# Optimization experiments

Hardware: AMD Instinct MI355X
Metric: run time of the kernel (lower is better)

Reference implementation:

```python
import jax, jax.numpy as jnp
import numpy as np
from jax import lax

# dims per init_kwargs / input_specs
V, D, N, W, B, T = 32000, 512, 250000, 64, 4, 1024
LOOPS, THRESH = 4, 0.99


def _ln(x, scale, bias):
    m = jnp.mean(x, -1, keepdims=True)
    v = jnp.var(x, -1, keepdims=True)
    return (x - m) * lax.rsqrt(v + 1e-5) * scale + bias


def setup_inputs() -> dict:
    key = jax.random.key(0)
    ks = jax.random.split(key, 12)
    s = 0.02
    p = lambda k, shape: jax.random.normal(k, shape, jnp.float32) * s
    return {
        "input_ids": jax.random.randint(ks[0], (B, T), 0, V),
        "embed": p(ks[1], (V, D)),
        "enc_w": p(ks[2], (D, D)), "enc_b": jnp.zeros((D,), jnp.float32),
        "ln_enc_s": jnp.ones((D,), jnp.float32), "ln_enc_b": jnp.zeros((D,), jnp.float32),
        "idx_w": p(ks[3], (D, D)), "idx_b": jnp.zeros((D,), jnp.float32),
        "mu_w": p(ks[4], (D, 1)), "mu_b": jnp.zeros((1,), jnp.float32),
        "sig_w": p(ks[5], (D, 1)), "sig_b": jnp.zeros((1,), jnp.float32),
        "pool_table": p(ks[6], (N, D)),
        "int_w1": p(ks[7], (2 * D, D)), "int_b1": jnp.zeros((D,), jnp.float32),
        "int_w2": p(ks[8], (D, D)), "int_b2": jnp.zeros((D,), jnp.float32),
        "ln_s": jnp.ones((D,), jnp.float32), "ln_b": jnp.zeros((D,), jnp.float32),
        "halt_w": p(ks[9], (D, 1)), "halt_b": jnp.zeros((1,), jnp.float32),
        "dec_w": p(ks[10], (D, V)), "dec_b": jnp.zeros((V,), jnp.float32),
    }


def reference(input_ids, embed, enc_w, enc_b, ln_enc_s, ln_enc_b,
              idx_w, idx_b, mu_w, mu_b, sig_w, sig_b, pool_table,
              int_w1, int_b1, int_w2, int_b2, ln_s, ln_b,
              halt_w, halt_b, dec_w, dec_b):
    # TinyController.encode: embed -> Dense -> gelu -> LayerNorm
    hidden = _ln(jax.nn.gelu(embed[input_ids] @ enc_w + enc_b), ln_enc_s, ln_enc_b)  # [B,T,D]
    state = hidden
    dt = hidden.dtype
    halt_prob = jnp.zeros((B, T, 1), dt)
    halted = jnp.zeros((B, T, 1), dt)
    idxs = []
    for _ in range(LOOPS):  # fixed small loop count, unrolled
        prev = state
        pooled = jnp.mean(state, axis=1)                       # [B,D]
        h = jax.nn.gelu(pooled @ idx_w + idx_b)
        mu = jax.nn.sigmoid(h @ mu_w + mu_b)                   # [B,1], coord in [0,1]
        sigma = jax.nn.softplus(h @ sig_w + sig_b) + 1e-4      # [B,1]
        # CoordinateMassivePool: contiguous window of W rows around mu*N
        center = mu[:, 0] * N
        start = jnp.clip(jnp.floor(center - W / 2).astype(jnp.int32), 0, N - W)  # [B]
        window = jax.vmap(lambda s: lax.dynamic_slice(pool_table, (s, 0), (W, D)))(start)  # [B,W,D]
        pos = (start[:, None] + jnp.arange(W)[None, :]).astype(dt) / N            # [B,W]
        w = jnp.exp(-0.5 * ((pos - mu) / sigma) ** 2)
        w = w / jnp.sum(w, axis=-1, keepdims=True)
        retrieved = jnp.einsum('bw,bwd->bd', w, window)        # [B,D]
        combined = jnp.concatenate(
            [state, jnp.broadcast_to(retrieved[:, None, :], (B, T, D))], axis=-1)  # [B,T,2D]
        integrated = _ln(jax.nn.gelu(combined @ int_w1 + int_b1) @ int_w2 + int_b2, ln_s, ln_b)
        candidate = state + integrated
        # ACT halting
        p_halt = jax.nn.sigmoid(candidate @ halt_w + halt_b)   # [B,T,1]
        halt_prob = halt_prob + p_halt * (1.0 - halted)
        new_halted = (halt_prob > THRESH).astype(dt)
        state = (1.0 - halted) * candidate + halted * prev
        halted = new_halted
        idxs.append(start)
    logits = state @ dec_w + dec_b                             # [B,T,V]
    all_indices = jnp.stack(idxs, axis=1)                      # [B,LOOPS]
    return logits, all_indices
```

## Files before the change

kernel.cpp:

```cpp
#include <hip/hip_runtime.h>

#define DEV __device__ __forceinline__

typedef __attribute__((ext_vector_type(8))) short bf16x8;
typedef __attribute__((ext_vector_type(4))) float f32x4;

typedef const __attribute__((address_space(1))) void* gsrc_t;
typedef __attribute__((address_space(3))) void* gdst_t;

DEV void gld16(const void* g, void* l){ __builtin_amdgcn_global_load_lds((gsrc_t)g,(gdst_t)l,16,0,0); }

DEV unsigned short f2bf(float f){
  union { float f; unsigned int u; } x; x.f = f;
  unsigned int u = x.u;
  return (unsigned short)((u + 0x7fffu + ((u >> 16) & 1u)) >> 16);
}
DEV unsigned long long pack4bf(float a, float b, float c, float d){
  return (unsigned long long)f2bf(a)
       | ((unsigned long long)f2bf(b) << 16)
       | ((unsigned long long)f2bf(c) << 32)
       | ((unsigned long long)f2bf(d) << 48);
}
DEV float gelu_t(float x){
  float u = 0.7978845608028654f * (x + 0.044715f * x * x * x);
  return 0.5f * x * (1.0f + tanhf(u));
}
DEV float sigmoidf_(float x){ return 1.0f / (1.0f + expf(-x)); }

DEV void BAR_TOP(){ __builtin_amdgcn_s_barrier(); asm volatile("" ::: "memory"); }
DEV void BAR_END(){
  __builtin_amdgcn_sched_barrier(0);
  asm volatile("s_waitcnt lgkmcnt(0)" ::: "memory");
  __builtin_amdgcn_s_barrier();
  asm volatile("" ::: "memory");
}

__global__ __launch_bounds__(256) void kPrep(const float* __restrict__ dec_w,
                                             unsigned short* __restrict__ dec_wT,
                                             const float* __restrict__ s0, const float* __restrict__ s1,
                                             const float* __restrict__ s2,
                                             unsigned short* __restrict__ d0, unsigned short* __restrict__ d1,
                                             unsigned short* __restrict__ d2,
                                             const int* __restrict__ ids,
                                             const float* __restrict__ embed,
                                             unsigned short* __restrict__ E){
  __shared__ float t[64][65];
  const int bid = blockIdx.x, tid = threadIdx.x;
  if (bid < 4000){
    int n0 = (bid % 500) * 64, k0 = (bid / 500) * 64;
    #pragma unroll
    for (int i = 0; i < 16; i++){
      int idx = i * 256 + tid; int r = idx >> 6, c = idx & 63;
      t[r][c] = dec_w[(size_t)(k0 + r) * 32000 + n0 + c];
    }
    __syncthreads();
    #pragma unroll
    for (int i = 0; i < 16; i++){
      int idx = i * 256 + tid; int r = idx >> 6, c = idx & 63;
      dec_wT[(size_t)(n0 + r) * 512 + k0 + c] = f2bf(t[c][r]);
    }
  } else if (bid < 4192){
    int rel = bid - 4000;
    int z = rel >> 6, rem = rel & 63;
    const float* W = (z == 0) ? s0 : (z == 1) ? s1 : s2;
    unsigned short* D = (z == 0) ? d0 : (z == 1) ? d1 : d2;
    int n0 = (rem & 7) * 64, k0 = (rem >> 3) * 64;
    #pragma unroll
    for (int i = 0; i < 16; i++){
      int idx = i * 256 + tid; int r = idx >> 6, c = idx & 63;
      t[r][c] = W[(size_t)(k0 + r) * 512 + n0 + c];
    }
    __syncthreads();
    #pragma unroll
    for (int i = 0; i < 16; i++){
      int idx = i * 256 + tid; int r = idx >> 6, c = idx & 63;
      D[(size_t)(n0 + r) * 512 + k0 + c] = f2bf(t[c][r]);
    }
  } else {
    int idx = bid - 4192;
    int row = idx * 2 + (tid >> 7);
    int t2  = tid & 127;
    int id = ids[row];
    float4 v = ((const float4*)(embed + (size_t)id * 512))[t2];
    *(unsigned long long*)(E + (size_t)row * 512 + t2 * 4) = pack4bf(v.x, v.y, v.z, v.w);
  }
}

template<int ENC>
__global__ __launch_bounds__(512) void kGemmLN(
    const unsigned short* __restrict__ A, const unsigned short* __restrict__ BT,
    const float* __restrict__ bias, const float* __restrict__ lns, const float* __restrict__ lnb,
    const float* __restrict__ hw, const float* __restrict__ hb,
    float* __restrict__ st, unsigned short* __restrict__ stb,
    float* __restrict__ part, float* __restrict__ halt_p, float* __restrict__ halted){
  __shared__ alignas(16) unsigned short lA[2][16 * 32];
  __shared__ alignas(16) unsigned short lB[2][512 * 32];
  __shared__ float pS[8][16], pQ[8][16], pH[8][16];
  __shared__ float sMean[16], sRs[16], sFac[16];
  const int tid = threadIdx.x, w = tid >> 6, lane = tid & 63;
  const int q = lane >> 4, c = lane & 15, lk8 = q * 8;
  const int r0 = blockIdx.x * 16;
  const int br = tid >> 2, bk = (tid & 3) * 8;
  f32x4 acc[4] = {};

  auto STAGE = [&](int buf, int k0){
    if (w == 0)
      gld16(A + (size_t)(r0 + (lane >> 2)) * 512 + k0 + (lane & 3) * 8, &lA[buf][lane * 8]);
    #pragma unroll
    for (int i = 0; i < 4; i++)
      gld16(BT + (size_t)(i * 128 + br) * 512 + k0 + bk, &lB[buf][(i * 512 + tid) * 8]);
  };

  STAGE(0, 0);
  #pragma unroll
  for (int t = 0; t < 16; t++){
    if (t < 15){
      STAGE((t + 1) & 1, (t + 1) * 32);
      if (w == 0) asm volatile("s_waitcnt vmcnt(5)" ::: "memory");
      else        asm volatile("s_waitcnt vmcnt(4)" ::: "memory");
    } else {
      asm volatile("s_waitcnt vmcnt(0)" ::: "memory");
    }
    BAR_TOP();
    bf16x8 af = *(const bf16x8*)&lA[t & 1][c * 32 + lk8];
    bf16x8 bfv[4];
    #pragma unroll
    for (int n = 0; n < 4; n++)
      bfv[n] = *(const bf16x8*)&lB[t & 1][(w * 64 + n * 16 + c) * 32 + lk8];
    #pragma unroll
    for (int n = 0; n < 4; n++)
      acc[n] = __builtin_amdgcn_mfma_f32_16x16x32_bf16(af, bfv[n], acc[n], 0, 0, 0);
    BAR_END();
  }

  #pragma unroll
  for (int n = 0; n < 4; n++){
    float bcol = bias[w * 64 + n * 16 + c];
    #pragma unroll
    for (int r = 0; r < 4; r++){
      float v = acc[n][r] + bcol;
      if (ENC) v = gelu_t(v);
      acc[n][r] = v;
    }
  }
  float rS[4], rQ[4];
  #pragma unroll
  for (int r = 0; r < 4; r++){
    float s = 0.f, s2 = 0.f;
    #pragma unroll
    for (int n = 0; n < 4; n++){ float v = acc[n][r]; s += v; s2 += v * v; }
    rS[r] = s; rQ[r] = s2;
  }
  #pragma unroll
  for (int mask = 1; mask < 16; mask <<= 1)
    #pragma unroll
    for (int r = 0; r < 4; r++){
      rS[r] += __shfl_xor(rS[r], mask);
      rQ[r] += __shfl_xor(rQ[r], mask);
    }
  if (c == 0)
    #pragma unroll
    for (int r = 0; r < 4; r++){ pS[w][q * 4 + r] = rS[r]; pQ[w][q * 4 + r] = rQ[r]; }
  __syncthreads();
  if (tid < 16){
    float s = 0.f, s2 = 0.f;
    #pragma unroll
    for (int v = 0; v < 8; v++){ s += pS[v][tid]; s2 += pQ[v][tid]; }
    float mean = s * (1.f / 512.f);
    float var  = s2 * (1.f / 512.f) - mean * mean;
    sMean[tid] = mean; sRs[tid] = rsqrtf(var + 1e-5f);
    if (ENC){ halt_p[r0 + tid] = 0.f; halted[r0 + tid] = 0.f; }
  }
  __syncthreads();
  float lnsv[4], lnbv[4];
  #pragma unroll
  for (int n = 0; n < 4; n++){ lnsv[n] = lns[w * 64 + n * 16 + c]; lnbv[n] = lnb[w * 64 + n * 16 + c]; }
  #pragma unroll
  for (int r = 0; r < 4; r++){
    int row = q * 4 + r;
    float mu = sMean[row], rs = sRs[row];
    #pragma unroll
    for (int n = 0; n < 4; n++)
      acc[n][r] = (acc[n][r] - mu) * rs * lnsv[n] + lnbv[n];
  }

  float sold[4][4];
  if (!ENC){
    float hwv[4];
    #pragma unroll
    for (int n = 0; n < 4; n++) hwv[n] = hw[w * 64 + n * 16 + c];
    #pragma unroll
    for (int r = 0; r < 4; r++){
      int row = q * 4 + r;
      #pragma unroll
      for (int n = 0; n < 4; n++)
        sold[n][r] = st[(size_t)(r0 + row) * 512 + w * 64 + n * 16 + c];
    }
    float rH[4];
    #pragma unroll
    for (int r = 0; r < 4; r++){
      float d = 0.f;
      #pragma unroll
      for (int n = 0; n < 4; n++) d += (sold[n][r] + acc[n][r]) * hwv[n];
      rH[r] = d;
    }
    #pragma unroll
    for (int mask = 1; mask < 16; mask <<= 1)
      #pragma unroll
      for (int r = 0; r < 4; r++) rH[r] += __shfl_xor(rH[r], mask);
    if (c == 0)
      #pragma unroll
      for (int r = 0; r < 4; r++) pH[w][q * 4 + r] = rH[r];
    __syncthreads();
    if (tid < 16){
      float d = 0.f;
      #pragma unroll
      for (int v = 0; v < 8; v++) d += pH[v][tid];
      float hd = halted[r0 + tid];
      float p  = sigmoidf_(d + hb[0]);
      float hp = halt_p[r0 + tid] + p * (1.f - hd);
      halt_p[r0 + tid] = hp;
      halted[r0 + tid] = (hp > 0.99f) ? 1.f : 0.f;
      sFac[tid] = 1.f - hd;
    }
    __syncthreads();
    #pragma unroll
    for (int r = 0; r < 4; r++){
      float f = sFac[q * 4 + r];
      #pragma unroll
      for (int n = 0; n < 4; n++)
        acc[n][r] = sold[n][r] + f * acc[n][r];
    }
  }

  #pragma unroll
  for (int r = 0; r < 4; r++){
    int row = r0 + q * 4 + r;
    #pragma unroll
    for (int n = 0; n < 4; n++){
      int col = w * 64 + n * 16 + c;
      float v = acc[n][r];
      st [(size_t)row * 512 + col] = v;
      stb[(size_t)row * 512 + col] = f2bf(v);
    }
  }
  #pragma unroll
  for (int n = 0; n < 4; n++){
    float s = 0.f;
    #pragma unroll
    for (int r = 0; r < 4; r++) s += acc[n][r];
    s += __shfl_xor(s, 16);
    s += __shfl_xor(s, 32);
    if (q == 0) part[(size_t)blockIdx.x * 512 + w * 64 + n * 16 + c] = s;
  }
}

__global__ __launch_bounds__(256) void kGemm64(const unsigned short* __restrict__ A,
                                               const unsigned short* __restrict__ BT,
                                               const float* __restrict__ rb,
                                               unsigned short* __restrict__ C){
  __shared__ alignas(16) unsigned short lA[2][64 * 32];
  __shared__ alignas(16) unsigned short lB[2][64 * 32];
  const int tid = threadIdx.x, w = tid >> 6, lane = tid & 63;
  const int q = lane >> 4, c = lane & 15, lk8 = q * 8;
  const int wm = w >> 1, wn = w & 1;
  const int m0 = blockIdx.y * 64, n0 = blockIdx.x * 64;
  const int sr = tid >> 2, sk = (tid & 3) * 8;
  f32x4 acc[2][2] = {};

  auto STAGE = [&](int buf, int k0){
    gld16(A  + (size_t)(m0 + sr) * 512 + k0 + sk, &lA[buf][tid * 8]);
    gld16(BT + (size_t)(n0 + sr) * 512 + k0 + sk, &lB[buf][tid * 8]);
  };

  STAGE(0, 0);
  #pragma unroll
  for (int t = 0; t < 16; t++){
    if (t < 15){
      STAGE((t + 1) & 1, (t + 1) * 32);
      asm volatile("s_waitcnt vmcnt(2)" ::: "memory");
    } else {
      asm volatile("s_waitcnt vmcnt(0)" ::: "memory");
    }
    BAR_TOP();
    bf16x8 af[2], bfv[2];
    #pragma unroll
    for (int m = 0; m < 2; m++) af[m]  = *(const bf16x8*)&lA[t & 1][(wm * 32 + m * 16 + c) * 32 + lk8];
    #pragma unroll
    for (int n = 0; n < 2; n++) bfv[n] = *(const bf16x8*)&lB[t & 1][(wn * 32 + n * 16 + c) * 32 + lk8];
    #pragma unroll
    for (int m = 0; m < 2; m++)
      #pragma unroll
      for (int n = 0; n < 2; n++)
        acc[m][n] = __builtin_amdgcn_mfma_f32_16x16x32_bf16(af[m], bfv[n], acc[m][n], 0, 0, 0);
    BAR_END();
  }

  #pragma unroll
  for (int m = 0; m < 2; m++)
    #pragma unroll
    for (int n = 0; n < 2; n++)
      #pragma unroll
      for (int r = 0; r < 4; r++){
        int row = m0 + wm * 32 + m * 16 + q * 4 + r;
        int col = n0 + wn * 32 + n * 16 + c;
        float v = acc[m][n][r] + rb[((row >> 10) << 9) + col];
        C[(size_t)row * 512 + col] = f2bf(gelu_t(v));
      }
}

__global__ __launch_bounds__(512) void kGemmDec(const unsigned short* __restrict__ A,
                                                const unsigned short* __restrict__ BT,
                                                const float* __restrict__ bias,
                                                float* __restrict__ C){
  __shared__ alignas(16) unsigned short lA[3][128 * 32];
  __shared__ alignas(16) unsigned short lB[3][256 * 32];
  const int tid = threadIdx.x, w = tid >> 6, lane = tid & 63;
  const int wm = w >> 2, wn = w & 3;
  const int c = lane & 15, q = lane >> 4;
  const int rk8 = (q ^ ((c >> 1) & 3)) * 8;
  int flat = blockIdx.x;
  flat = (flat & 7) * 500 + (flat >> 3);
  const int m0 = (flat & 31) * 128;
  const int n0 = (flat >> 5) * 256;
  const int srow  = tid >> 2;
  const int skoff = ((tid & 3) ^ ((srow >> 1) & 3)) * 8;
  const int sdst  = srow * 32 + (tid & 3) * 8;
  f32x4 acc[4][4] = {};

  auto STAGE = [&](int buf, int k0){
    gld16(A  + (size_t)(m0 + srow) * 512 + k0 + skoff,       &lA[buf][sdst]);
    gld16(BT + (size_t)(n0 + srow) * 512 + k0 + skoff,       &lB[buf][sdst]);
    gld16(BT + (size_t)(n0 + 128 + srow) * 512 + k0 + skoff, &lB[buf][128 * 32 + sdst]);
  };

  STAGE(0, 0);
  STAGE(1, 32);
  for (int t = 0; t < 16; t++){
    const int buf = t % 3;
    if (t < 15) asm volatile("s_waitcnt vmcnt(3)" ::: "memory");
    else        asm volatile("s_waitcnt vmcnt(0)" ::: "memory");
    __builtin_amdgcn_s_barrier();
    asm volatile("" ::: "memory");
    bf16x8 af[4], bfr[4];
    #pragma unroll
    for (int mf = 0; mf < 4; mf++)
      af[mf] = *(const bf16x8*)&lA[buf][(wm * 64 + mf * 16 + c) * 32 + rk8];
    #pragma unroll
    for (int nf = 0; nf < 4; nf++)
      bfr[nf] = *(const bf16x8*)&lB[buf][(wn * 64 + nf * 16 + c) * 32 + rk8];
    if (t < 14) STAGE((t + 2) % 3, (t + 2) * 32);
    asm volatile("s_waitcnt lgkmcnt(0)" ::: "memory");
    __builtin_amdgcn_sched_barrier(0);
    __builtin_amdgcn_s_setprio(1);
    #pragma unroll
    for (int mf = 0; mf < 4; mf++)
      #pragma unroll
      for (int nf = 0; nf < 4; nf++)
        acc[mf][nf] = __builtin_amdgcn_mfma_f32_16x16x32_bf16(af[mf], bfr[nf], acc[mf][nf], 0, 0, 0);
    __builtin_amdgcn_s_setprio(0);
  }

  #pragma unroll
  for (int mf = 0; mf < 4; mf++){
    int rbase = m0 + wm * 64 + mf * 16 + q * 4;
    #pragma unroll
    for (int nf = 0; nf < 4; nf++){
      int col = n0 + wn * 64 + nf * 16 + c;
      float bcol = bias[col];
      #pragma unroll
      for (int r = 0; r < 4; r++)
        __builtin_nontemporal_store(acc[mf][nf][r] + bcol,
                                    &C[(size_t)(rbase + r) * 32000 + col]);
    }
  }
}

__global__ __launch_bounds__(512) void kCtl(const float* __restrict__ part,
                                            const float* __restrict__ idx_w, const float* __restrict__ idx_b,
                                            const float* __restrict__ mu_w, const float* __restrict__ mu_b,
                                            const float* __restrict__ sig_w, const float* __restrict__ sig_b,
                                            const float* __restrict__ pool_table,
                                            const float* __restrict__ w1b, const float* __restrict__ int_b1,
                                            float* __restrict__ r2, float* __restrict__ outIdx, int loop){
  __shared__ float xs[512];
  __shared__ float red[512];
  __shared__ float red2[512];
  __shared__ float evals[64];
  __shared__ float sc[4];
  int b = blockIdx.x, tid = threadIdx.x;

  float s = 0.f;
  #pragma unroll 8
  for (int c2 = 0; c2 < 64; c2++) s += part[(size_t)(b * 64 + c2) * 512 + tid];
  xs[tid] = s * (1.0f / 1024.0f);
  __syncthreads();

  float a = idx_b[tid];
  #pragma unroll 16
  for (int i = 0; i < 512; i++)
    a = fmaf(xs[i], idx_w[(size_t)i * 512 + tid], a);
  float hv = gelu_t(a);
  red[tid]  = hv * mu_w[tid];
  red2[tid] = hv * sig_w[tid];
  __syncthreads();
  for (int off2 = 256; off2 > 0; off2 >>= 1){
    if (tid < off2){ red[tid] += red[tid + off2]; red2[tid] += red2[tid + off2]; }
    __syncthreads();
  }
  if (tid == 0){
    float mu = sigmoidf_(red[0] + mu_b[0]);
    float sg = log1pf(expf(red2[0] + sig_b[0])) + 1e-4f;
    float center = mu * 250000.0f;
    int stt = (int)floorf(center - 32.0f);
    stt = stt < 0 ? 0 : (stt > 250000 - 64 ? 250000 - 64 : stt);
    sc[0] = mu; sc[1] = sg; sc[2] = (float)stt;
    outIdx[b * 4 + loop] = (float)stt;
  }
  __syncthreads();
  if (tid < 64){
    float pos = (sc[2] + (float)tid) * (1.0f / 250000.0f);
    float z = (pos - sc[0]) / sc[1];
    evals[tid] = expf(-0.5f * z * z);
  }
  __syncthreads();
  if (tid == 0){
    float wsum = 0.f;
    for (int j = 0; j < 64; j++) wsum += evals[j];
    sc[3] = wsum;
  }
  __syncthreads();
  int stt = (int)sc[2];
  float r = 0.f;
  #pragma unroll 8
  for (int j = 0; j < 64; j++)
    r = fmaf(evals[j], pool_table[(size_t)(stt + j) * 512 + tid], r);
  r /= sc[3];
  __syncthreads();
  xs[tid] = r;
  __syncthreads();
  float a2 = int_b1[tid];
  #pragma unroll 16
  for (int i = 0; i < 512; i++)
    a2 = fmaf(xs[i], w1b[(size_t)i * 512 + tid], a2);
  r2[(size_t)b * 512 + tid] = a2;
}

extern "C" void kernel_launch(void* const* d_in, const int* in_sizes, int n_in,
                              void* d_out, int out_size, void* d_ws, size_t ws_size,
                              hipStream_t stream){
  (void)in_sizes; (void)n_in; (void)out_size; (void)ws_size;
  const int*   ids    = (const int*)  d_in[0];
  const float* embed  = (const float*)d_in[1];
  const float* enc_w  = (const float*)d_in[2];
  const float* enc_b  = (const float*)d_in[3];
  const float* ln_es  = (const float*)d_in[4];
  const float* ln_eb  = (const float*)d_in[5];
  const float* idx_w  = (const float*)d_in[6];
  const float* idx_b  = (const float*)d_in[7];
  const float* mu_w   = (const float*)d_in[8];
  const float* mu_b   = (const float*)d_in[9];
  const float* sig_w  = (const float*)d_in[10];
  const float* sig_b  = (const float*)d_in[11];
  const float* pool_t = (const float*)d_in[12];
  const float* int_w1 = (const float*)d_in[13];
  const float* int_b1 = (const float*)d_in[14];
  const float* int_w2 = (const float*)d_in[15];
  const float* int_b2 = (const float*)d_in[16];
  const float* ln_s   = (const float*)d_in[17];
  const float* ln_b   = (const float*)d_in[18];
  const float* halt_w = (const float*)d_in[19];
  const float* halt_b = (const float*)d_in[20];
  const float* dec_w  = (const float*)d_in[21];
  const float* dec_b  = (const float*)d_in[22];

  char* ws = (char*)d_ws;
  size_t off = 0;
  auto alloc = [&](size_t bytes)->char*{
    char* p = ws + off; off += (bytes + 255) & ~(size_t)255; return p;
  };
  unsigned short* dec_wT  = (unsigned short*)alloc(32000ull * 512 * 2);
  unsigned short* enc_wT  = (unsigned short*)alloc(512ull * 512 * 2);
  unsigned short* w1T     = (unsigned short*)alloc(512ull * 512 * 2);
  unsigned short* w2T     = (unsigned short*)alloc(512ull * 512 * 2);
  unsigned short* bufB    = (unsigned short*)alloc(4096ull * 512 * 2);
  float*          state   = (float*)alloc(4096ull * 512 * 4);
  unsigned short* state_b = (unsigned short*)alloc(4096ull * 512 * 2);
  float*          part    = (float*)alloc(256ull * 512 * 4);
  float*          r2      = (float*)alloc(4ull * 512 * 4);
  float*          halt_p  = (float*)alloc(4096 * 4);
  float*          halted  = (float*)alloc(4096 * 4);
  float*          outF    = (float*)d_out;

  hipLaunchKernelGGL(kPrep, dim3(6240), dim3(256), 0, stream,
                     dec_w, dec_wT, enc_w, int_w1, int_w2, enc_wT, w1T, w2T,
                     ids, embed, bufB);

  hipLaunchKernelGGL((kGemmLN<1>), dim3(256), dim3(512), 0, stream,
                     bufB, enc_wT, enc_b, ln_es, ln_eb,
                     (const float*)nullptr, (const float*)nullptr,
                     state, state_b, part, halt_p, halted);

  for (int l = 0; l < 4; l++){
    hipLaunchKernelGGL(kCtl, dim3(4), dim3(512), 0, stream, part, idx_w, idx_b,
                       mu_w, mu_b, sig_w, sig_b, pool_t,
                       int_w1 + 512 * 512, int_b1,
                       r2, outF + 131072000, l);
    hipLaunchKernelGGL(kGemm64, dim3(8, 64), dim3(256), 0, stream,
                       state_b, w1T, r2, bufB);
    hipLaunchKernelGGL((kGemmLN<0>), dim3(256), dim3(512), 0, stream,
                       bufB, w2T, int_b2, ln_s, ln_b, halt_w, halt_b,
                       state, state_b, part, halt_p, halted);
  }

  hipLaunchKernelGGL(kGemmDec, dim3(4000), dim3(512), 0, stream,
                     state_b, dec_wT, dec_b, (float*)d_out);
}
```

Baseline: 501.4 us.

## Fuse controller into first integration GEMM with flag-based overlap

Result: slower. 1.540 ms (+207.2%).

```diff
diff --git a/kernel.cpp b/kernel.cpp
--- a/kernel.cpp
+++ b/kernel.cpp
@@ -43,9 +43,11 @@
                                              unsigned short* __restrict__ d2,
                                              const int* __restrict__ ids,
                                              const float* __restrict__ embed,
-                                             unsigned short* __restrict__ E){
+                                             unsigned short* __restrict__ E,
+                                             unsigned int* __restrict__ flag){
   __shared__ float t[64][65];
   const int bid = blockIdx.x, tid = threadIdx.x;
+  if (bid == 0 && tid < 16) flag[tid] = 0u;
   if (bid < 4000){
     int n0 = (bid % 500) * 64, k0 = (bid / 500) * 64;
     #pragma unroll
@@ -255,16 +257,105 @@
   }
 }
 
-__global__ __launch_bounds__(256) void kGemm64(const unsigned short* __restrict__ A,
-                                               const unsigned short* __restrict__ BT,
-                                               const float* __restrict__ rb,
-                                               unsigned short* __restrict__ C){
+__global__ __launch_bounds__(256) void kGemm64C(const unsigned short* __restrict__ A,
+                                                const unsigned short* __restrict__ BT,
+                                                float* __restrict__ r2,
+                                                unsigned short* __restrict__ C,
+                                                const float* __restrict__ part,
+                                                const float* __restrict__ idx_w, const float* __restrict__ idx_b,
+                                                const float* __restrict__ mu_w, const float* __restrict__ mu_b,
+                                                const float* __restrict__ sig_w, const float* __restrict__ sig_b,
+                                                const float* __restrict__ pool_table,
+                                                const float* __restrict__ w1b, const float* __restrict__ int_b1,
+                                                unsigned int* __restrict__ flag,
+                                                float* __restrict__ outIdx, int l){
+  const int bid = blockIdx.x, tid = threadIdx.x;
+
+  if (bid < 4){
+    __shared__ float xs[512], red[512], red2[512], evals[64], sc[4];
+    const int b = bid;
+    float s0 = 0.f, s1 = 0.f;
+    #pragma unroll 8
+    for (int c2 = 0; c2 < 64; c2++){
+      s0 += part[(size_t)(b * 64 + c2) * 512 + tid];
+      s1 += part[(size_t)(b * 64 + c2) * 512 + tid + 256];
+    }
+    xs[tid] = s0 * (1.0f / 1024.0f);
+    xs[tid + 256] = s1 * (1.0f / 1024.0f);
+    __syncthreads();
+    float a0 = idx_b[tid], a1 = idx_b[tid + 256];
+    #pragma unroll 16
+    for (int i = 0; i < 512; i++){
+      float x = xs[i];
+      a0 = fmaf(x, idx_w[(size_t)i * 512 + tid], a0);
+      a1 = fmaf(x, idx_w[(size_t)i * 512 + tid + 256], a1);
+    }
+    float h0 = gelu_t(a0), h1 = gelu_t(a1);
+    red[tid]  = h0 * mu_w[tid]  + h1 * mu_w[tid + 256];
+    red2[tid] = h0 * sig_w[tid] + h1 * sig_w[tid + 256];
+    __syncthreads();
+    for (int off2 = 128; off2 > 0; off2 >>= 1){
+      if (tid < off2){ red[tid] += red[tid + off2]; red2[tid] += red2[tid + off2]; }
+      __syncthreads();
+    }
+    if (tid == 0){
+      float mu = sigmoidf_(red[0] + mu_b[0]);
+      float sg = log1pf(expf(red2[0] + sig_b[0])) + 1e-4f;
+      float center = mu * 250000.0f;
+      int stt = (int)floorf(center - 32.0f);
+      stt = stt < 0 ? 0 : (stt > 250000 - 64 ? 250000 - 64 : stt);
+      sc[0] = mu; sc[1] = sg; sc[2] = (float)stt;
+      outIdx[b * 4 + l] = (float)stt;
+    }
+    __syncthreads();
+    if (tid < 64){
+      float pos = (sc[2] + (float)tid) * (1.0f / 250000.0f);
+      float z = (pos - sc[0]) / sc[1];
+      evals[tid] = expf(-0.5f * z * z);
+    }
+    __syncthreads();
+    if (tid == 0){
+      float ws = 0.f;
+      for (int j = 0; j < 64; j++) ws += evals[j];
+      sc[3] = ws;
+    }
+    __syncthreads();
+    int stt = (int)sc[2];
+    float r0v = 0.f, r1v = 0.f;
+    #pragma unroll 8
+    for (int j = 0; j < 64; j++){
+      float e = evals[j];
+      r0v = fmaf(e, pool_table[(size_t)(stt + j) * 512 + tid], r0v);
+      r1v = fmaf(e, pool_table[(size_t)(stt + j) * 512 + tid + 256], r1v);
+    }
+    r0v /= sc[3]; r1v /= sc[3];
+    __syncthreads();
+    xs[tid] = r0v; xs[tid + 256] = r1v;
+    __syncthreads();
+    float a20 = int_b1[tid], a21 = int_b1[tid + 256];
+    #pragma unroll 16
+    for (int i = 0; i < 512; i++){
+      float x = xs[i];
+      a20 = fmaf(x, w1b[(size_t)i * 512 + tid], a20);
+      a21 = fmaf(x, w1b[(size_t)i * 512 + tid + 256], a21);
+    }
+    r2[(size_t)b * 512 + tid] = a20;
+    r2[(size_t)b * 512 + tid + 256] = a21;
+    __threadfence();
+    __syncthreads();
+    if (tid == 0)
+      __hip_atomic_exchange(&flag[l * 4 + b], 1u, __ATOMIC_RELEASE, __HIP_MEMORY_SCOPE_AGENT);
+    return;
+  }
+
   __shared__ alignas(16) unsigned short lA[2][64 * 32];
   __shared__ alignas(16) unsigned short lB[2][64 * 32];
-  const int tid = threadIdx.x, w = tid >> 6, lane = tid & 63;
+  const int g = bid - 4;
+  const int w = tid >> 6, lane = tid & 63;
   const int q = lane >> 4, c = lane & 15, lk8 = q * 8;
   const int wm = w >> 1, wn = w & 1;
-  const int m0 = blockIdx.y * 64, n0 = blockIdx.x * 64;
+  const int m0 = (g >> 3) * 64, n0 = (g & 7) * 64;
+  const int b = g >> 7;
   const int sr = tid >> 2, sk = (tid & 3) * 8;
   f32x4 acc[2][2] = {};
 
@@ -296,6 +387,13 @@
     BAR_END();
   }
 
+  if (tid == 0){
+    while (__hip_atomic_fetch_add(&flag[l * 4 + b], 0u, __ATOMIC_ACQUIRE,
+                                  __HIP_MEMORY_SCOPE_AGENT) == 0u)
+      __builtin_amdgcn_s_sleep(16);
+  }
+  __syncthreads();
+
   #pragma unroll
   for (int m = 0; m < 2; m++)
     #pragma unroll
@@ -304,7 +402,7 @@
       for (int r = 0; r < 4; r++){
         int row = m0 + wm * 32 + m * 16 + q * 4 + r;
         int col = n0 + wn * 32 + n * 16 + c;
-        float v = acc[m][n][r] + rb[((row >> 10) << 9) + col];
+        float v = acc[m][n][r] + r2[((row >> 10) << 9) + col];
         C[(size_t)row * 512 + col] = f2bf(gelu_t(v));
       }
 }
@@ -342,6 +440,7 @@
     else        asm volatile("s_waitcnt vmcnt(0)" ::: "memory");
     __builtin_amdgcn_s_barrier();
     asm volatile("" ::: "memory");
+    if (t < 14) STAGE((t + 2) % 3, (t + 2) * 32);
     bf16x8 af[4], bfr[4];
     #pragma unroll
     for (int mf = 0; mf < 4; mf++)
@@ -349,9 +448,6 @@
     #pragma unroll
     for (int nf = 0; nf < 4; nf++)
       bfr[nf] = *(const bf16x8*)&lB[buf][(wn * 64 + nf * 16 + c) * 32 + rk8];
-    if (t < 14) STAGE((t + 2) % 3, (t + 2) * 32);
-    asm volatile("s_waitcnt lgkmcnt(0)" ::: "memory");
-    __builtin_amdgcn_sched_barrier(0);
     __builtin_amdgcn_s_setprio(1);
     #pragma unroll
     for (int mf = 0; mf < 4; mf++)
@@ -374,76 +470,6 @@
                                     &C[(size_t)(rbase + r) * 32000 + col]);
     }
   }
-}
-
-__global__ __launch_bounds__(512) void kCtl(const float* __restrict__ part,
-                                            const float* __restrict__ idx_w, const float* __restrict__ idx_b,
-                                            const float* __restrict__ mu_w, const float* __restrict__ mu_b,
-                                            const float* __restrict__ sig_w, const float* __restrict__ sig_b,
-                                            const float* __restrict__ pool_table,
-                                            const float* __restrict__ w1b, const float* __restrict__ int_b1,
-                                            float* __restrict__ r2, float* __restrict__ outIdx, int loop){
-  __shared__ float xs[512];
-  __shared__ float red[512];
-  __shared__ float red2[512];
-  __shared__ float evals[64];
-  __shared__ float sc[4];
-  int b = blockIdx.x, tid = threadIdx.x;
-
-  float s = 0.f;
-  #pragma unroll 8
-  for (int c2 = 0; c2 < 64; c2++) s += part[(size_t)(b * 64 + c2) * 512 + tid];
-  xs[tid] = s * (1.0f / 1024.0f);
-  __syncthreads();
-
-  float a = idx_b[tid];
-  #pragma unroll 16
-  for (int i = 0; i < 512; i++)
-    a = fmaf(xs[i], idx_w[(size_t)i * 512 + tid], a);
-  float hv = gelu_t(a);
-  red[tid]  = hv * mu_w[tid];
-  red2[tid] = hv * sig_w[tid];
-  __syncthreads();
-  for (int off2 = 256; off2 > 0; off2 >>= 1){
-    if (tid < off2){ red[tid] += red[tid + off2]; red2[tid] += red2[tid + off2]; }
-    __syncthreads();
-  }
-  if (tid == 0){
-    float mu = sigmoidf_(red[0] + mu_b[0]);
-    float sg = log1pf(expf(red2[0] + sig_b[0])) + 1e-4f;
-    float center = mu * 250000.0f;
-    int stt = (int)floorf(center - 32.0f);
-    stt = stt < 0 ? 0 : (stt > 250000 - 64 ? 250000 - 64 : stt);
-    sc[0] = mu; sc[1] = sg; sc[2] = (float)stt;
-    outIdx[b * 4 + loop] = (float)stt;
-  }
-  __syncthreads();
-  if (tid < 64){
-    float pos = (sc[2] + (float)tid) * (1.0f / 250000.0f);
-    float z = (pos - sc[0]) / sc[1];
-    evals[tid] = expf(-0.5f * z * z);
-  }
-  __syncthreads();
-  if (tid == 0){
-    float wsum = 0.f;
-    for (int j = 0; j < 64; j++) wsum += evals[j];
-    sc[3] = wsum;
-  }
-  __syncthreads();
-  int stt = (int)sc[2];
-  float r = 0.f;
-  #pragma unroll 8
-  for (int j = 0; j < 64; j++)
-    r = fmaf(evals[j], pool_table[(size_t)(stt + j) * 512 + tid], r);
-  r /= sc[3];
-  __syncthreads();
-  xs[tid] = r;
-  __syncthreads();
-  float a2 = int_b1[tid];
-  #pragma unroll 16
-  for (int i = 0; i < 512; i++)
-    a2 = fmaf(xs[i], w1b[(size_t)i * 512 + tid], a2);
-  r2[(size_t)b * 512 + tid] = a2;
 }
 
 extern "C" void kernel_launch(void* const* d_in, const int* in_sizes, int n_in,
@@ -490,11 +516,13 @@
   float*          r2      = (float*)alloc(4ull * 512 * 4);
   float*          halt_p  = (float*)alloc(4096 * 4);
   float*          halted  = (float*)alloc(4096 * 4);
+  unsigned int*   flag    = (unsigned int*)alloc(16 * 4);
   float*          outF    = (float*)d_out;
+  const float*    w1b     = int_w1 + 512 * 512;
 
   hipLaunchKernelGGL(kPrep, dim3(6240), dim3(256), 0, stream,
                      dec_w, dec_wT, enc_w, int_w1, int_w2, enc_wT, w1T, w2T,
-                     ids, embed, bufB);
+                     ids, embed, bufB, flag);
 
   hipLaunchKernelGGL((kGemmLN<1>), dim3(256), dim3(512), 0, stream,
                      bufB, enc_wT, enc_b, ln_es, ln_eb,
@@ -502,12 +530,10 @@
                      state, state_b, part, halt_p, halted);
 
   for (int l = 0; l < 4; l++){
-    hipLaunchKernelGGL(kCtl, dim3(4), dim3(512), 0, stream, part, idx_w, idx_b,
-                       mu_w, mu_b, sig_w, sig_b, pool_t,
-                       int_w1 + 512 * 512, int_b1,
-                       r2, outF + 131072000, l);
-    hipLaunchKernelGGL(kGemm64, dim3(8, 64), dim3(256), 0, stream,
-                       state_b, w1T, r2, bufB);
+    hipLaunchKernelGGL(kGemm64C, dim3(516), dim3(256), 0, stream,
+                       state_b, w1T, r2, bufB, part,
+                       idx_w, idx_b, mu_w, mu_b, sig_w, sig_b, pool_t,
+                       w1b, int_b1, flag, outF + 131072000, l);
     hipLaunchKernelGGL((kGemmLN<0>), dim3(256), dim3(512), 0, stream,
                        bufB, w2T, int_b2, ln_s, ln_b, halt_w, halt_b,
                        state, state_b, part, halt_p, halted);
```
